# Performance work log

Measured on AMD Instinct MI355X. Metric: run time of the kernel, lower is better.

Reference implementation:

```python
import jax, jax.numpy as jnp
import numpy as np

DIM = 10  # GMM components == feature dim


def _conv(x, w, b):
    y = jax.lax.conv_general_dilated(x, w, window_strides=(1, 1), padding='VALID',
                                     dimension_numbers=('NCHW', 'OIHW', 'NCHW'))
    return y + b[None, :, None, None]


def _gmm(x, centers, raw_mats):
    # x: [B, d]; centers: [K, d]; raw_mats: [K, d, d] with K == d == DIM
    K, d = centers.shape
    I = jnp.eye(d, dtype=x.dtype)
    L = jnp.tril(raw_mats, -1) + I                       # unit lower-triangular [K,d,d]
    root_D = jnp.diagonal(raw_mats, axis1=-2, axis2=-1)  # [K,d]
    D = root_D * root_D + 1e-4
    # Sigma_inv = L^{-T} D^{-1} L^{-1}
    L_inv = jax.scipy.linalg.solve_triangular(L, jnp.broadcast_to(I, L.shape), lower=True)
    Sigma_inv = jnp.einsum('kai,ka,kaj->kij', L_inv, 1.0 / D, L_inv)
    det_scale = jax.lax.rsqrt(jnp.prod(D, axis=-1))      # [K]
    diff = x[:, None, :] - centers[None, :, :]           # [B,K,d]
    dist_sq = jnp.einsum('bkd,kde,bke->bk', diff, Sigma_inv, diff)
    expo = -0.5 * dist_sq
    expo_safe = expo - jnp.max(expo, axis=1, keepdims=True)
    numer = det_scale[None, :] * jnp.exp(expo_safe)
    return numer / jnp.sum(numer, axis=1, keepdims=True)


def setup_inputs() -> dict:
    key = jax.random.key(0)
    ks = jax.random.split(key, 12)
    B = 4096
    x = jax.random.normal(ks[0], (B, 1, 28, 28), dtype=jnp.float32)
    conv1_w = jax.random.normal(ks[1], (32, 1, 3, 3), jnp.float32) * (1.0 / np.sqrt(1 * 9))
    conv1_b = jnp.zeros((32,), jnp.float32)
    conv2_w = jax.random.normal(ks[2], (64, 32, 3, 3), jnp.float32) * (1.0 / np.sqrt(32 * 9))
    conv2_b = jnp.zeros((64,), jnp.float32)
    fc1_w = jax.random.normal(ks[3], (128, 9216), jnp.float32) * (1.0 / np.sqrt(9216))
    fc1_b = jnp.zeros((128,), jnp.float32)
    fc2_w = jax.random.normal(ks[4], (DIM, 128), jnp.float32) * (1.0 / np.sqrt(128))
    fc2_b = jnp.zeros((DIM,), jnp.float32)
    centers = jax.random.normal(ks[5], (DIM, DIM), jnp.float32)
    raw_mats = jax.random.normal(ks[6], (DIM, DIM, DIM), jnp.float32) * 0.1 + jnp.eye(DIM)[None]
    return {'x': x, 'conv1_w': conv1_w, 'conv1_b': conv1_b, 'conv2_w': conv2_w,
            'conv2_b': conv2_b, 'fc1_w': fc1_w, 'fc1_b': fc1_b, 'fc2_w': fc2_w,
            'fc2_b': fc2_b, 'centers': centers, 'raw_mats': raw_mats}


def reference(x, conv1_w, conv1_b, conv2_w, conv2_b, fc1_w, fc1_b, fc2_w, fc2_b, centers, raw_mats):
    h = jax.nn.relu(_conv(x, conv1_w, conv1_b))          # [B,32,26,26]
    h = jax.nn.relu(_conv(h, conv2_w, conv2_b))          # [B,64,24,24]
    h = jax.lax.reduce_window(h, -jnp.inf, jax.lax.max, (1, 1, 2, 2), (1, 1, 2, 2), 'VALID')
    h = h.reshape(h.shape[0], -1)                        # [B,9216] (dropout = identity in eval)
    h = jax.nn.relu(h @ fc1_w.T + fc1_b)
    h = h @ fc2_w.T + fc2_b                              # [B,10]
    return _gmm(h, centers, raw_mats)
```

## Files before the change

### kernel.cpp

```cpp
#include <hip/hip_runtime.h>

typedef _Float16 half_t;
typedef _Float16 half8  __attribute__((ext_vector_type(8)));
typedef _Float16 half2v __attribute__((ext_vector_type(2)));
typedef float    floatx4 __attribute__((ext_vector_type(4)));

#define MFMA16(a, b, c) __builtin_amdgcn_mfma_f32_16x16x32_f16((a), (b), (c), 0, 0, 0)

__global__ void k_prep(const float* __restrict__ fw1, half_t* __restrict__ W1h,
                       const float* __restrict__ w2, half_t* __restrict__ W2T,
                       const float* __restrict__ raw, float* __restrict__ Sinv,
                       float* __restrict__ dets) {
    __shared__ float s_raw[1000];
    __shared__ float s_Li[1000];
    __shared__ float s_Dinv[100];
    const int blk = blockIdx.x;
    const int t = threadIdx.x;
    if (blk < 4608) {
        const int i = blk * 256 + t;
        W1h[i] = (half_t)fw1[i];
    } else if (blk < 4680) {
        const int i = (blk - 4608) * 256 + t;
        if (i < 18432) {
            const int tap = i / 2048;
            const int r = i - tap * 2048;
            const int co = r >> 5;
            const int ci = r & 31;
            W2T[i] = (half_t)w2[(co * 32 + ci) * 9 + tap];
        }
    } else {
        for (int i = t; i < 1000; i += 256) s_raw[i] = raw[i];
        __syncthreads();
        if (t < 100) {
            const int k = t / 10;
            const int j = t - k * 10;
            float v[10];
#pragma unroll
            for (int i = 0; i < 10; ++i) {
                float s = (i == j) ? 1.0f : 0.0f;
#pragma unroll
                for (int mm = 0; mm < 10; ++mm)
                    if (mm < i) s -= s_raw[k * 100 + i * 10 + mm] * v[mm];
                v[i] = s;
            }
#pragma unroll
            for (int a = 0; a < 10; ++a) s_Li[k * 100 + a * 10 + j] = v[a];
        } else if (t < 110) {
            const int k = t - 100;
            float prod = 1.0f;
#pragma unroll
            for (int a = 0; a < 10; ++a) {
                const float rd = s_raw[k * 100 + a * 10 + a];
                const float dv = rd * rd + 1e-4f;
                s_Dinv[k * 10 + a] = 1.0f / dv;
                prod *= dv;
            }
            dets[k] = rsqrtf(prod);
        }
        __syncthreads();
        for (int idx = t; idx < 1000; idx += 256) {
            const int k = idx / 100;
            const int r = idx - k * 100;
            const int ii = r / 10;
            const int jj = r - ii * 10;
            float s = 0.0f;
#pragma unroll
            for (int a = 0; a < 10; ++a)
                s += s_Li[k * 100 + a * 10 + ii] * s_Dinv[k * 10 + a] *
                     s_Li[k * 100 + a * 10 + jj];
            Sinv[idx] = s;
        }
    }
}

__global__ __launch_bounds__(256, 3) void k_convs(
    const float* __restrict__ x, const float* __restrict__ w1,
    const float* __restrict__ b1, const float* __restrict__ b2,
    const half_t* __restrict__ W2T, half_t* __restrict__ h2p) {
    __shared__ float s_x[784];
    __shared__ float s_w1[288];
    __shared__ float s_b1[32];
    __shared__ float s_b2[64];
    __shared__ __align__(16) half_t s_h1[688 * 32];

    const int t = threadIdx.x;
    const int b = blockIdx.x;

    for (int i = t; i < 784; i += 256) s_x[i] = x[(size_t)b * 784 + i];
    for (int i = t; i < 288; i += 256) s_w1[i] = w1[i];
    if (t < 32) s_b1[t] = b1[t];
    if (t < 64) s_b2[t] = b2[t];
    if (t < 384) s_h1[21632 + t] = (half_t)0.0f;
    __syncthreads();

    const int w = t >> 6;
    const int ln = t & 63;
    const int n16 = ln & 15;
    const int q = ln >> 4;

    {
        float wr[8][9], br[8];
#pragma unroll
        for (int j = 0; j < 8; ++j) {
            br[j] = s_b1[w * 8 + j];
#pragma unroll
            for (int k = 0; k < 9; ++k) wr[j][k] = s_w1[(w * 8 + j) * 9 + k];
        }
        for (int p = ln; p < 676; p += 64) {
            const int yy = p / 26;
            const int xx = p - yy * 26;
            float win[9];
#pragma unroll
            for (int r = 0; r < 3; ++r)
#pragma unroll
                for (int c = 0; c < 3; ++c) win[r * 3 + c] = s_x[(yy + r) * 28 + xx + c];
            half8 hv;
#pragma unroll
            for (int j = 0; j < 8; ++j) {
                float a = br[j];
#pragma unroll
                for (int k = 0; k < 9; ++k) a = fmaf(win[k], wr[j][k], a);
                hv[j] = (half_t)fmaxf(a, 0.0f);
            }
            *(half8*)((char*)s_h1 + ((p << 6) + (w << 4))) = hv;
        }
    }

    const int cp = w & 1;
    const int st = w >> 1;
    half8 bf[9][2];
#pragma unroll
    for (int tap = 0; tap < 9; ++tap)
#pragma unroll
        for (int cc = 0; cc < 2; ++cc)
            bf[tap][cc] = *(const half8*)(W2T +
                ((tap * 64 + (2 * cp + cc) * 16 + n16) * 32 + q * 8));

    __syncthreads();

#pragma unroll
    for (int tap = 0; tap < 9; ++tap)
#pragma unroll
        for (int cc = 0; cc < 2; ++cc)
            asm volatile("" : "+v"(bf[tap][cc]));

    const char* rp = (const char*)s_h1 + (((n16 + 16 * st) << 6) + (q << 4));

    const float bb0 = s_b2[cp * 32 + n16];
    const float bb1 = s_b2[cp * 32 + 16 + n16];
    half_t* outp = h2p + (size_t)b * 9216 + (size_t)(cp * 32 + n16) * 144 +
                   8 * st + 2 * q;
    const bool dostore = (st == 0) | (q < 2);

    const floatx4 z4 = {0.f, 0.f, 0.f, 0.f};
    floatx4 sl0[2] = {z4, z4}, sl1[2] = {z4, z4}, sl2[2] = {z4, z4};
    float yb00 = 0.f, yb01 = 0.f, yb10 = 0.f, yb11 = 0.f;

#define RETIRE(YO, AC)                                                        \
    do {                                                                      \
        const float p0 = fmaxf(AC[0][0], AC[0][1]);                           \
        const float p1 = fmaxf(AC[0][2], AC[0][3]);                           \
        const float r0 = fmaxf(AC[1][0], AC[1][1]);                           \
        const float r1 = fmaxf(AC[1][2], AC[1][3]);                           \
        if (((YO) & 1) == 0) {                                                \
            yb00 = p0; yb01 = p1; yb10 = r0; yb11 = r1;                       \
        } else if (dostore) {                                                 \
            half2v h0, h1v;                                                   \
            h0[0] = (half_t)fmaxf(fmaxf(yb00, p0) + bb0, 0.0f);               \
            h0[1] = (half_t)fmaxf(fmaxf(yb01, p1) + bb0, 0.0f);               \
            h1v[0] = (half_t)fmaxf(fmaxf(yb10, r0) + bb1, 0.0f);              \
            h1v[1] = (half_t)fmaxf(fmaxf(yb11, r1) + bb1, 0.0f);              \
            half_t* op = outp + ((YO) >> 1) * 12;                             \
            *(half2v*)(op) = h0;                                              \
            *(half2v*)(op + 2304) = h1v;                                      \
        }                                                                     \
        AC[0] = z4; AC[1] = z4;                                               \
    } while (0)

#define CSTEP(Y_, A0, A1, A2)                                                 \
    do {                                                                      \
        const int y_ = (Y_);                                                  \
        if (y_ < 26) {                                                        \
            const half8 f0 = *(const half8*)(rp);                             \
            const half8 f1 = *(const half8*)(rp + 64);                        \
            const half8 f2 = *(const half8*)(rp + 128);                       \
            if (y_ <= 23) {                 \
                A0[0] = MFMA16(f0, bf[0][0], A0[0]);                          \
                A0[1] = MFMA16(f0, bf[0][1], A0[1]);                          \
                A0[0] = MFMA16(f1, bf[1][0], A0[0]);                          \
                A0[1] = MFMA16(f1, bf[1][1], A0[1]);                          \
                A0[0] = MFMA16(f2, bf[2][0], A0[0]);                          \
                A0[1] = MFMA16(f2, bf[2][1], A0[1]);                          \
            }                                                                 \
            if (y_ >= 1 && y_ <= 24) {    \
                A1[0] = MFMA16(f0, bf[3][0], A1[0]);                          \
                A1[1] = MFMA16(f0, bf[3][1], A1[1]);                          \
                A1[0] = MFMA16(f1, bf[4][0], A1[0]);                          \
                A1[1] = MFMA16(f1, bf[4][1], A1[1]);                          \
                A1[0] = MFMA16(f2, bf[5][0], A1[0]);                          \
                A1[1] = MFMA16(f2, bf[5][1], A1[1]);                          \
            }                                                                 \
            if (y_ >= 2) {   \
                A2[0] = MFMA16(f0, bf[6][0], A2[0]);                          \
                A2[1] = MFMA16(f0, bf[6][1], A2[1]);                          \
                A2[0] = MFMA16(f1, bf[7][0], A2[0]);                          \
                A2[1] = MFMA16(f1, bf[7][1], A2[1]);                          \
                A2[0] = MFMA16(f2, bf[8][0], A2[0]);                          \
                A2[1] = MFMA16(f2, bf[8][1], A2[1]);                          \
                RETIRE(y_ - 2, A2);                                           \
            }                                                                 \
            rp += 1664;                                                       \
        }                                                                     \
    } while (0)

    for (int yb = 0; yb < 27; yb += 3) {
        CSTEP(yb + 0, sl0, sl2, sl1);
        CSTEP(yb + 1, sl1, sl0, sl2);
        CSTEP(yb + 2, sl2, sl1, sl0);
    }
#undef CSTEP
#undef RETIRE
}

__global__ __launch_bounds__(256) void k_fc1(const half_t* __restrict__ A,
                                             const half_t* __restrict__ W,
                                             half_t* __restrict__ part) {
    const int t = threadIdx.x;
    const int mb = blockIdx.x;
    const int kb = blockIdx.y;
    const int w = t >> 6, ln = t & 63, n16 = ln & 15, q = ln >> 4;

    const half_t* a0 = A + (size_t)(mb * 64 + w * 16 + n16) * 9216 + kb * 576 + q * 8;
    const half_t* wp = W + (size_t)n16 * 9216 + kb * 576 + q * 8;

    floatx4 acc[8];
#pragma unroll
    for (int nt = 0; nt < 8; ++nt) acc[nt] = (floatx4){0.f, 0.f, 0.f, 0.f};

#pragma unroll 2
    for (int kt = 0; kt < 18; ++kt) {
        const int ko = kt * 32;
        half8 af = *(const half8*)(a0 + ko);
#pragma unroll
        for (int nt = 0; nt < 8; ++nt) {
            half8 bfr = *(const half8*)(wp + (size_t)nt * 16 * 9216 + ko);
            acc[nt] = MFMA16(af, bfr, acc[nt]);
        }
    }
    const int rowbase = mb * 64 + w * 16;
#pragma unroll
    for (int nt = 0; nt < 8; ++nt)
#pragma unroll
        for (int r = 0; r < 4; ++r) {
            const int row = rowbase + q * 4 + r;
            const int col = nt * 16 + n16;
            part[(size_t)kb * 524288 + (size_t)row * 128 + col] = (half_t)acc[nt][r];
        }
}

__global__ __launch_bounds__(64) void k_tail(
    const half_t* __restrict__ part, const float* __restrict__ fb1,
    const float* __restrict__ fw, const float* __restrict__ fb,
    const float* __restrict__ cent, const float* __restrict__ Sinv,
    const float* __restrict__ dets, float* __restrict__ out) {
    __shared__ float sw[1280];
    __shared__ float sfb1[128];
    __shared__ float sb[10];
    __shared__ float sc[100];
    __shared__ float ss[1000];
    __shared__ float sd[10];
    const int t = threadIdx.x;
    for (int i = t; i < 1280; i += 64) sw[i] = fw[i];
    for (int i = t; i < 128; i += 64) sfb1[i] = fb1[i];
    if (t < 10) sb[t] = fb[t];
    for (int i = t; i < 100; i += 64) sc[i] = cent[i];
    for (int i = t; i < 1000; i += 64) ss[i] = Sinv[i];
    if (t < 10) sd[t] = dets[t];
    __syncthreads();

    const int smp = blockIdx.x * 64 + t;
    const half_t* ps = part + (size_t)smp * 128;

    float y[10];
#pragma unroll
    for (int o = 0; o < 10; ++o) y[o] = sb[o];

#pragma unroll
    for (int g = 0; g < 4; ++g) {
        float acc[32];
#pragma unroll
        for (int c = 0; c < 32; ++c) acc[c] = 0.0f;
#pragma unroll
        for (int kb = 0; kb < 16; ++kb) {
            const half8* pk = (const half8*)(ps + (size_t)kb * 524288 + g * 32);
#pragma unroll
            for (int vv = 0; vv < 4; ++vv) {
                const half8 v = pk[vv];
#pragma unroll
                for (int j = 0; j < 8; ++j) acc[vv * 8 + j] += (float)v[j];
            }
        }
#pragma unroll
        for (int c = 0; c < 32; ++c) {
            const half_t hv = (half_t)fmaxf(acc[c] + sfb1[g * 32 + c], 0.0f);
            const float hf = (float)hv;
#pragma unroll
            for (int o = 0; o < 10; ++o)
                y[o] = fmaf(hf, sw[o * 128 + g * 32 + c], y[o]);
        }
    }

    float expo[10];
    float mx = -3.402823466e38f;
#pragma unroll
    for (int k = 0; k < 10; ++k) {
        float d[10];
#pragma unroll
        for (int j = 0; j < 10; ++j) d[j] = y[j] - sc[k * 10 + j];
        float s = 0.0f;
#pragma unroll
        for (int i = 0; i < 10; ++i) {
            float r = 0.0f;
#pragma unroll
            for (int j = 0; j < 10; ++j) r = fmaf(ss[k * 100 + i * 10 + j], d[j], r);
            s = fmaf(d[i], r, s);
        }
        expo[k] = -0.5f * s;
        mx = fmaxf(mx, expo[k]);
    }
    float num[10];
    float sum = 0.0f;
#pragma unroll
    for (int k = 0; k < 10; ++k) {
        num[k] = sd[k] * __expf(expo[k] - mx);
        sum += num[k];
    }
    const float inv = 1.0f / sum;
#pragma unroll
    for (int k = 0; k < 10; ++k) out[(size_t)smp * 10 + k] = num[k] * inv;
}

extern "C" void kernel_launch(void* const* d_in, const int* in_sizes, int n_in,
                              void* d_out, int out_size, void* d_ws, size_t ws_size,
                              hipStream_t stream) {
    const float* x = (const float*)d_in[0];
    const float* w1 = (const float*)d_in[1];
    const float* b1 = (const float*)d_in[2];
    const float* w2 = (const float*)d_in[3];
    const float* b2 = (const float*)d_in[4];
    const float* fw1 = (const float*)d_in[5];
    const float* fb1 = (const float*)d_in[6];
    const float* fw2 = (const float*)d_in[7];
    const float* fb2 = (const float*)d_in[8];
    const float* cen = (const float*)d_in[9];
    const float* raw = (const float*)d_in[10];
    float* out = (float*)d_out;

    char* ws = (char*)d_ws;
    half_t* W2T = (half_t*)(ws);
    half_t* W1h = (half_t*)(ws + 36864);
    half_t* h2p = (half_t*)(ws + 2396160);
    half_t* part = (half_t*)(ws + 77893632);
    float* gS = (float*)(ws + 95719424);
    float* gD = (float*)(ws + 95723424);

    k_prep<<<4681, 256, 0, stream>>>(fw1, W1h, w2, W2T, raw, gS, gD);
    k_convs<<<4096, 256, 0, stream>>>(x, w1, b1, b2, W2T, h2p);
    k_fc1<<<dim3(64, 16), 256, 0, stream>>>(h2p, W1h, part);
    k_tail<<<64, 64, 0, stream>>>(part, fb1, fw2, fb2, cen, gS, gD, out);
}
```

Baseline: 292.9 us.

## Software-pipeline conv2 row loads and double fc1 rows per wave

The conv2 row loop now issues the next input row's loads before the current row's MFMAs, using double-buffered fragments, and peels the last two rows so the boundary branches are compile-time. This aims to hide LDS or global load latency behind MFMA work. Separately, each fc1 wave now computes 32 rows instead of 16, reusing every weight fragment across two A tiles and halving the grid. That raises register pressure and cuts the number of blocks in flight.

```diff
diff --git a/kernel.cpp b/kernel.cpp
--- a/kernel.cpp
+++ b/kernel.cpp
@@ -177,48 +177,83 @@
         AC[0] = z4; AC[1] = z4;                                               \
     } while (0)
 
-#define CSTEP(Y_, A0, A1, A2)                                                 \
+#define CLOADN(F0, F1, F2)                                                    \
     do {                                                                      \
-        const int y_ = (Y_);                                                  \
-        if (y_ < 26) {                                                        \
-            const half8 f0 = *(const half8*)(rp);                             \
-            const half8 f1 = *(const half8*)(rp + 64);                        \
-            const half8 f2 = *(const half8*)(rp + 128);                       \
-            if (y_ <= 23) {                 \
-                A0[0] = MFMA16(f0, bf[0][0], A0[0]);                          \
-                A0[1] = MFMA16(f0, bf[0][1], A0[1]);                          \
-                A0[0] = MFMA16(f1, bf[1][0], A0[0]);                          \
-                A0[1] = MFMA16(f1, bf[1][1], A0[1]);                          \
-                A0[0] = MFMA16(f2, bf[2][0], A0[0]);                          \
-                A0[1] = MFMA16(f2, bf[2][1], A0[1]);                          \
-            }                                                                 \
-            if (y_ >= 1 && y_ <= 24) {    \
-                A1[0] = MFMA16(f0, bf[3][0], A1[0]);                          \
-                A1[1] = MFMA16(f0, bf[3][1], A1[1]);                          \
-                A1[0] = MFMA16(f1, bf[4][0], A1[0]);                          \
-                A1[1] = MFMA16(f1, bf[4][1], A1[1]);                          \
-                A1[0] = MFMA16(f2, bf[5][0], A1[0]);                          \
-                A1[1] = MFMA16(f2, bf[5][1], A1[1]);                          \
-            }                                                                 \
-            if (y_ >= 2) {   \
-                A2[0] = MFMA16(f0, bf[6][0], A2[0]);                          \
-                A2[1] = MFMA16(f0, bf[6][1], A2[1]);                          \
-                A2[0] = MFMA16(f1, bf[7][0], A2[0]);                          \
-                A2[1] = MFMA16(f1, bf[7][1], A2[1]);                          \
-                A2[0] = MFMA16(f2, bf[8][0], A2[0]);                          \
-                A2[1] = MFMA16(f2, bf[8][1], A2[1]);                          \
-                RETIRE(y_ - 2, A2);                                           \
-            }                                                                 \
-            rp += 1664;                                                       \
+        F0 = *(const half8*)(rp);                                             \
+        F1 = *(const half8*)(rp + 64);                                        \
+        F2 = *(const half8*)(rp + 128);                                       \
+        rp += 1664;                                                           \
+    } while (0)
+
+#define CWORK(Y_, F0, F1, F2, A0, A1, A2)                                     \
+    do {                                                                      \
+        A0[0] = MFMA16(F0, bf[0][0], A0[0]);                                  \
+        A0[1] = MFMA16(F0, bf[0][1], A0[1]);                                  \
+        A0[0] = MFMA16(F1, bf[1][0], A0[0]);                                  \
+        A0[1] = MFMA16(F1, bf[1][1], A0[1]);                                  \
+        A0[0] = MFMA16(F2, bf[2][0], A0[0]);                                  \
+        A0[1] = MFMA16(F2, bf[2][1], A0[1]);                                  \
+        if ((Y_) >= 1) {                                                      \
+            A1[0] = MFMA16(F0, bf[3][0], A1[0]);                              \
+            A1[1] = MFMA16(F0, bf[3][1], A1[1]);                              \
+            A1[0] = MFMA16(F1, bf[4][0], A1[0]);                              \
+            A1[1] = MFMA16(F1, bf[4][1], A1[1]);                              \
+            A1[0] = MFMA16(F2, bf[5][0], A1[0]);                              \
+            A1[1] = MFMA16(F2, bf[5][1], A1[1]);                              \
+        }                                                                     \
+        if ((Y_) >= 2) {                                                      \
+            A2[0] = MFMA16(F0, bf[6][0], A2[0]);                              \
+            A2[1] = MFMA16(F0, bf[6][1], A2[1]);                              \
+            A2[0] = MFMA16(F1, bf[7][0], A2[0]);                              \
+            A2[1] = MFMA16(F1, bf[7][1], A2[1]);                              \
+            A2[0] = MFMA16(F2, bf[8][0], A2[0]);                              \
+            A2[1] = MFMA16(F2, bf[8][1], A2[1]);                              \
+            RETIRE((Y_) - 2, A2);                                             \
         }                                                                     \
     } while (0)
 
-    for (int yb = 0; yb < 27; yb += 3) {
-        CSTEP(yb + 0, sl0, sl2, sl1);
-        CSTEP(yb + 1, sl1, sl0, sl2);
-        CSTEP(yb + 2, sl2, sl1, sl0);
-    }
-#undef CSTEP
+    half8 fa0, fa1, fa2, fb0, fb1, fb2;
+    CLOADN(fa0, fa1, fa2);
+
+    for (int yb = 0; yb < 24; yb += 6) {
+        CLOADN(fb0, fb1, fb2);
+        CWORK(yb + 0, fa0, fa1, fa2, sl0, sl2, sl1);
+        CLOADN(fa0, fa1, fa2);
+        CWORK(yb + 1, fb0, fb1, fb2, sl1, sl0, sl2);
+        CLOADN(fb0, fb1, fb2);
+        CWORK(yb + 2, fa0, fa1, fa2, sl2, sl1, sl0);
+        CLOADN(fa0, fa1, fa2);
+        CWORK(yb + 3, fb0, fb1, fb2, sl0, sl2, sl1);
+        CLOADN(fb0, fb1, fb2);
+        CWORK(yb + 4, fa0, fa1, fa2, sl1, sl0, sl2);
+        CLOADN(fa0, fa1, fa2);
+        CWORK(yb + 5, fb0, fb1, fb2, sl2, sl1, sl0);
+    }
+    CLOADN(fb0, fb1, fb2);
+    {
+        sl2[0] = MFMA16(fa0, bf[3][0], sl2[0]);
+        sl2[1] = MFMA16(fa0, bf[3][1], sl2[1]);
+        sl2[0] = MFMA16(fa1, bf[4][0], sl2[0]);
+        sl2[1] = MFMA16(fa1, bf[4][1], sl2[1]);
+        sl2[0] = MFMA16(fa2, bf[5][0], sl2[0]);
+        sl2[1] = MFMA16(fa2, bf[5][1], sl2[1]);
+        sl1[0] = MFMA16(fa0, bf[6][0], sl1[0]);
+        sl1[1] = MFMA16(fa0, bf[6][1], sl1[1]);
+        sl1[0] = MFMA16(fa1, bf[7][0], sl1[0]);
+        sl1[1] = MFMA16(fa1, bf[7][1], sl1[1]);
+        sl1[0] = MFMA16(fa2, bf[8][0], sl1[0]);
+        sl1[1] = MFMA16(fa2, bf[8][1], sl1[1]);
+        RETIRE(22, sl1);
+        sl2[0] = MFMA16(fb0, bf[6][0], sl2[0]);
+        sl2[1] = MFMA16(fb0, bf[6][1], sl2[1]);
+        sl2[0] = MFMA16(fb1, bf[7][0], sl2[0]);
+        sl2[1] = MFMA16(fb1, bf[7][1], sl2[1]);
+        sl2[0] = MFMA16(fb2, bf[8][0], sl2[0]);
+        sl2[1] = MFMA16(fb2, bf[8][1], sl2[1]);
+        RETIRE(23, sl2);
+    }
+#undef CWORK
+#undef CLOADN
 #undef RETIRE
 }
 
@@ -230,32 +265,39 @@
     const int kb = blockIdx.y;
     const int w = t >> 6, ln = t & 63, n16 = ln & 15, q = ln >> 4;
 
-    const half_t* a0 = A + (size_t)(mb * 64 + w * 16 + n16) * 9216 + kb * 576 + q * 8;
+    const half_t* a0 = A + (size_t)(mb * 128 + w * 32 + n16) * 9216 + kb * 576 + q * 8;
+    const half_t* a1 = a0 + (size_t)16 * 9216;
     const half_t* wp = W + (size_t)n16 * 9216 + kb * 576 + q * 8;
 
-    floatx4 acc[8];
-#pragma unroll
-    for (int nt = 0; nt < 8; ++nt) acc[nt] = (floatx4){0.f, 0.f, 0.f, 0.f};
+    floatx4 acc[2][8];
+#pragma unroll
+    for (int s = 0; s < 2; ++s)
+#pragma unroll
+        for (int nt = 0; nt < 8; ++nt) acc[s][nt] = (floatx4){0.f, 0.f, 0.f, 0.f};
 
 #pragma unroll 2
     for (int kt = 0; kt < 18; ++kt) {
         const int ko = kt * 32;
-        half8 af = *(const half8*)(a0 + ko);
+        half8 af0 = *(const half8*)(a0 + ko);
+        half8 af1 = *(const half8*)(a1 + ko);
 #pragma unroll
         for (int nt = 0; nt < 8; ++nt) {
             half8 bfr = *(const half8*)(wp + (size_t)nt * 16 * 9216 + ko);
-            acc[nt] = MFMA16(af, bfr, acc[nt]);
-        }
-    }
-    const int rowbase = mb * 64 + w * 16;
-#pragma unroll
-    for (int nt = 0; nt < 8; ++nt)
-#pragma unroll
-        for (int r = 0; r < 4; ++r) {
-            const int row = rowbase + q * 4 + r;
-            const int col = nt * 16 + n16;
-            part[(size_t)kb * 524288 + (size_t)row * 128 + col] = (half_t)acc[nt][r];
-        }
+            acc[0][nt] = MFMA16(af0, bfr, acc[0][nt]);
+            acc[1][nt] = MFMA16(af1, bfr, acc[1][nt]);
+        }
+    }
+    const int rowbase = mb * 128 + w * 32;
+#pragma unroll
+    for (int s = 0; s < 2; ++s)
+#pragma unroll
+        for (int nt = 0; nt < 8; ++nt)
+#pragma unroll
+            for (int r = 0; r < 4; ++r) {
+                const int row = rowbase + s * 16 + q * 4 + r;
+                const int col = nt * 16 + n16;
+                part[(size_t)kb * 524288 + (size_t)row * 128 + col] = (half_t)acc[s][nt][r];
+            }
 }
 
 __global__ __launch_bounds__(64) void k_tail(
@@ -366,6 +408,6 @@
 
     k_prep<<<4681, 256, 0, stream>>>(fw1, W1h, w2, W2T, raw, gS, gD);
     k_convs<<<4096, 256, 0, stream>>>(x, w1, b1, b2, W2T, h2p);
-    k_fc1<<<dim3(64, 16), 256, 0, stream>>>(h2p, W1h, part);
+    k_fc1<<<dim3(32, 16), 256, 0, stream>>>(h2p, W1h, part);
     k_tail<<<64, 64, 0, stream>>>(part, fb1, fw2, fb2, cen, gS, gD, out);
 }
```

Measured after the change: 252.9 us. -13.6%, faster.

## Split conv kernel into half-image blocks and double fc1 rows per wave

Applied to the files above, without the earlier changes.

The fused conv kernel now processes half an image per block (two blocks per image), computing 14 conv1 rows with a halo and 12 conv2 output rows each, which cuts shared memory per block and doubles the grid. This is meant to raise occupancy and parallelism at the cost of recomputing two overlapping conv1 rows. The fc1 GEMM now has each wave compute two 16-row M tiles that share each loaded weight fragment, halving the weight reloads, with half as many blocks. The conv step loop is also fully unrolled.

```diff
diff --git a/kernel.cpp b/kernel.cpp
--- a/kernel.cpp
+++ b/kernel.cpp
@@ -77,20 +77,21 @@
     const float* __restrict__ x, const float* __restrict__ w1,
     const float* __restrict__ b1, const float* __restrict__ b2,
     const half_t* __restrict__ W2T, half_t* __restrict__ h2p) {
-    __shared__ float s_x[784];
+    __shared__ float s_x[448];
     __shared__ float s_w1[288];
     __shared__ float s_b1[32];
     __shared__ float s_b2[64];
-    __shared__ __align__(16) half_t s_h1[688 * 32];
+    __shared__ __align__(16) half_t s_h1[376 * 32];
 
     const int t = threadIdx.x;
-    const int b = blockIdx.x;
-
-    for (int i = t; i < 784; i += 256) s_x[i] = x[(size_t)b * 784 + i];
+    const int img = blockIdx.x >> 1;
+    const int yh = blockIdx.x & 1;
+
+    for (int i = t; i < 448; i += 256) s_x[i] = x[(size_t)img * 784 + yh * 336 + i];
     for (int i = t; i < 288; i += 256) s_w1[i] = w1[i];
     if (t < 32) s_b1[t] = b1[t];
     if (t < 64) s_b2[t] = b2[t];
-    if (t < 384) s_h1[21632 + t] = (half_t)0.0f;
+    for (int i = t; i < 384; i += 256) s_h1[11648 + i] = (half_t)0.0f;
     __syncthreads();
 
     const int w = t >> 6;
@@ -106,14 +107,14 @@
 #pragma unroll
             for (int k = 0; k < 9; ++k) wr[j][k] = s_w1[(w * 8 + j) * 9 + k];
         }
-        for (int p = ln; p < 676; p += 64) {
-            const int yy = p / 26;
-            const int xx = p - yy * 26;
+        for (int p = ln; p < 364; p += 64) {
+            const int ly = p / 26;
+            const int xx = p - ly * 26;
             float win[9];
 #pragma unroll
             for (int r = 0; r < 3; ++r)
 #pragma unroll
-                for (int c = 0; c < 3; ++c) win[r * 3 + c] = s_x[(yy + r) * 28 + xx + c];
+                for (int c = 0; c < 3; ++c) win[r * 3 + c] = s_x[(ly + r) * 28 + xx + c];
             half8 hv;
 #pragma unroll
             for (int j = 0; j < 8; ++j) {
@@ -148,8 +149,8 @@
 
     const float bb0 = s_b2[cp * 32 + n16];
     const float bb1 = s_b2[cp * 32 + 16 + n16];
-    half_t* outp = h2p + (size_t)b * 9216 + (size_t)(cp * 32 + n16) * 144 +
-                   8 * st + 2 * q;
+    half_t* outp = h2p + (size_t)img * 9216 + (size_t)(cp * 32 + n16) * 144 +
+                   yh * 72 + 8 * st + 2 * q;
     const bool dostore = (st == 0) | (q < 2);
 
     const floatx4 z4 = {0.f, 0.f, 0.f, 0.f};
@@ -177,14 +178,13 @@
         AC[0] = z4; AC[1] = z4;                                               \
     } while (0)
 
-#define CSTEP(Y_, A0, A1, A2)                                                 \
+#define CSTEP(S_, A0, A1, A2)                                                 \
     do {                                                                      \
-        const int y_ = (Y_);                                                  \
-        if (y_ < 26) {                                                        \
+        if ((S_) < 14) {                                                      \
             const half8 f0 = *(const half8*)(rp);                             \
             const half8 f1 = *(const half8*)(rp + 64);                        \
             const half8 f2 = *(const half8*)(rp + 128);                       \
-            if (y_ <= 23) {                 \
+            if ((S_) <= 11) {              \
                 A0[0] = MFMA16(f0, bf[0][0], A0[0]);                          \
                 A0[1] = MFMA16(f0, bf[0][1], A0[1]);                          \
                 A0[0] = MFMA16(f1, bf[1][0], A0[0]);                          \
@@ -192,7 +192,7 @@
                 A0[0] = MFMA16(f2, bf[2][0], A0[0]);                          \
                 A0[1] = MFMA16(f2, bf[2][1], A0[1]);                          \
             }                                                                 \
-            if (y_ >= 1 && y_ <= 24) {    \
+            if ((S_) >= 1 && (S_) <= 12) {       \
                 A1[0] = MFMA16(f0, bf[3][0], A1[0]);                          \
                 A1[1] = MFMA16(f0, bf[3][1], A1[1]);                          \
                 A1[0] = MFMA16(f1, bf[4][0], A1[0]);                          \
@@ -200,20 +200,21 @@
                 A1[0] = MFMA16(f2, bf[5][0], A1[0]);                          \
                 A1[1] = MFMA16(f2, bf[5][1], A1[1]);                          \
             }                                                                 \
-            if (y_ >= 2) {   \
+            if ((S_) >= 2) {        \
                 A2[0] = MFMA16(f0, bf[6][0], A2[0]);                          \
                 A2[1] = MFMA16(f0, bf[6][1], A2[1]);                          \
                 A2[0] = MFMA16(f1, bf[7][0], A2[0]);                          \
                 A2[1] = MFMA16(f1, bf[7][1], A2[1]);                          \
                 A2[0] = MFMA16(f2, bf[8][0], A2[0]);                          \
                 A2[1] = MFMA16(f2, bf[8][1], A2[1]);                          \
-                RETIRE(y_ - 2, A2);                                           \
+                RETIRE((S_) - 2, A2);                                         \
             }                                                                 \
             rp += 1664;                                                       \
         }                                                                     \
     } while (0)
 
-    for (int yb = 0; yb < 27; yb += 3) {
+#pragma unroll
+    for (int yb = 0; yb < 15; yb += 3) {
         CSTEP(yb + 0, sl0, sl2, sl1);
         CSTEP(yb + 1, sl1, sl0, sl2);
         CSTEP(yb + 2, sl2, sl1, sl0);
@@ -230,32 +231,39 @@
     const int kb = blockIdx.y;
     const int w = t >> 6, ln = t & 63, n16 = ln & 15, q = ln >> 4;
 
-    const half_t* a0 = A + (size_t)(mb * 64 + w * 16 + n16) * 9216 + kb * 576 + q * 8;
+    const half_t* a0 = A + (size_t)(mb * 128 + w * 32 + n16) * 9216 + kb * 576 + q * 8;
+    const half_t* a1 = a0 + (size_t)16 * 9216;
     const half_t* wp = W + (size_t)n16 * 9216 + kb * 576 + q * 8;
 
-    floatx4 acc[8];
-#pragma unroll
-    for (int nt = 0; nt < 8; ++nt) acc[nt] = (floatx4){0.f, 0.f, 0.f, 0.f};
+    floatx4 acc[2][8];
+#pragma unroll
+    for (int s = 0; s < 2; ++s)
+#pragma unroll
+        for (int nt = 0; nt < 8; ++nt) acc[s][nt] = (floatx4){0.f, 0.f, 0.f, 0.f};
 
 #pragma unroll 2
     for (int kt = 0; kt < 18; ++kt) {
         const int ko = kt * 32;
-        half8 af = *(const half8*)(a0 + ko);
+        half8 af0 = *(const half8*)(a0 + ko);
+        half8 af1 = *(const half8*)(a1 + ko);
 #pragma unroll
         for (int nt = 0; nt < 8; ++nt) {
             half8 bfr = *(const half8*)(wp + (size_t)nt * 16 * 9216 + ko);
-            acc[nt] = MFMA16(af, bfr, acc[nt]);
-        }
-    }
-    const int rowbase = mb * 64 + w * 16;
-#pragma unroll
-    for (int nt = 0; nt < 8; ++nt)
-#pragma unroll
-        for (int r = 0; r < 4; ++r) {
-            const int row = rowbase + q * 4 + r;
-            const int col = nt * 16 + n16;
-            part[(size_t)kb * 524288 + (size_t)row * 128 + col] = (half_t)acc[nt][r];
-        }
+            acc[0][nt] = MFMA16(af0, bfr, acc[0][nt]);
+            acc[1][nt] = MFMA16(af1, bfr, acc[1][nt]);
+        }
+    }
+    const int rowbase = mb * 128 + w * 32;
+#pragma unroll
+    for (int s = 0; s < 2; ++s)
+#pragma unroll
+        for (int nt = 0; nt < 8; ++nt)
+#pragma unroll
+            for (int r = 0; r < 4; ++r) {
+                const int row = rowbase + s * 16 + q * 4 + r;
+                const int col = nt * 16 + n16;
+                part[(size_t)kb * 524288 + (size_t)row * 128 + col] = (half_t)acc[s][nt][r];
+            }
 }
 
 __global__ __launch_bounds__(64) void k_tail(
@@ -365,7 +373,7 @@
     float* gD = (float*)(ws + 95723424);
 
     k_prep<<<4681, 256, 0, stream>>>(fw1, W1h, w2, W2T, raw, gS, gD);
-    k_convs<<<4096, 256, 0, stream>>>(x, w1, b1, b2, W2T, h2p);
-    k_fc1<<<dim3(64, 16), 256, 0, stream>>>(h2p, W1h, part);
+    k_convs<<<8192, 256, 0, stream>>>(x, w1, b1, b2, W2T, h2p);
+    k_fc1<<<dim3(32, 16), 256, 0, stream>>>(h2p, W1h, part);
     k_tail<<<64, 64, 0, stream>>>(part, fb1, fw2, fb2, cen, gS, gD, out);
 }
```

Result: faster. 264.3 us (-9.8%).
